# Kernel tuning notes

Hardware: AMD Instinct MI355X
Metric: run time of the kernel (lower is better)

## Reference

```python
import jax, jax.numpy as jnp
import numpy as np

N_NODES = 50000
N_EDGES = 800000
INPUT_DIM = 128
HIDDEN = 128
EMB = 64
OUT_DIM = 4


def gcn_norm(src, dst, w, num_nodes):
    """PyG gcn_norm: add self-loops (fill 1.0), sym-normalize D^-1/2 A D^-1/2."""
    loop = jnp.arange(num_nodes)
    src = jnp.concatenate([src, loop])
    dst = jnp.concatenate([dst, loop])
    w = jnp.concatenate([w, jnp.ones(num_nodes, w.dtype)])
    deg = jax.ops.segment_sum(w, dst, num_segments=num_nodes)
    dinv = jnp.where(deg > 0, jax.lax.rsqrt(jnp.where(deg > 0, deg, 1.0)), 0.0)
    return src, dst, dinv[src] * w * dinv[dst]


def propagate(h, src, dst, norm, num_nodes):
    # gather-scale-scatter-add: out[dst] += norm * h[src]
    return jax.ops.segment_sum(norm[:, None] * h[src], dst, num_segments=num_nodes)


def setup_inputs() -> dict:
    key = jax.random.key(0)
    ks = jax.random.split(key, 16)
    x = jax.random.normal(ks[0], (N_NODES, INPUT_DIM), dtype=jnp.float32)
    edge_index = jax.random.randint(ks[1], (2, N_EDGES), 0, N_NODES)
    edge_in = jax.random.randint(ks[2], (2, N_EDGES), 0, N_NODES)
    edge_out = jax.random.randint(ks[3], (2, N_EDGES), 0, N_NODES)
    in_w = jax.random.uniform(ks[4], (N_EDGES,), dtype=jnp.float32)
    out_w = jax.random.uniform(ks[5], (N_EDGES,), dtype=jnp.float32)
    # linear weights (bias=False), torch Linear stores [out, in]
    W0 = jax.random.normal(ks[6], (HIDDEN, INPUT_DIM), dtype=jnp.float32) / np.sqrt(INPUT_DIM)
    W1 = jax.random.normal(ks[7], (HIDDEN, HIDDEN * 3), dtype=jnp.float32) / np.sqrt(HIDDEN * 3)
    W2 = jax.random.normal(ks[8], (EMB, HIDDEN * 3), dtype=jnp.float32) / np.sqrt(HIDDEN * 3)
    b0 = jax.random.normal(ks[9], (1, HIDDEN), dtype=jnp.float32) * 0.01
    b1 = jax.random.normal(ks[10], (1, HIDDEN), dtype=jnp.float32) * 0.01
    b2 = jax.random.normal(ks[11], (1, EMB), dtype=jnp.float32) * 0.01
    # Conv1d(emb*3 -> out_dim, kernel=1) == pointwise linear
    Wc = jax.random.normal(ks[12], (OUT_DIM, EMB * 3), dtype=jnp.float32) / np.sqrt(EMB * 3)
    bc = jax.random.normal(ks[13], (OUT_DIM,), dtype=jnp.float32) * 0.01
    return {"x": x, "edge_index": edge_index, "edge_in": edge_in, "edge_out": edge_out,
            "in_w": in_w, "out_w": out_w, "W0": W0, "W1": W1, "W2": W2,
            "b0": b0, "b1": b1, "b2": b2, "Wc": Wc, "bc": bc}


def reference(x, edge_index, edge_in, edge_out, in_w, out_w,
              W0, W1, W2, b0, b1, b2, Wc, bc):
    n = x.shape[0]
    ones_w = jnp.ones(edge_index.shape[1], x.dtype)
    g1 = gcn_norm(edge_index[0], edge_index[1], ones_w, n)
    g2 = gcn_norm(edge_in[0], edge_in[1], in_w, n)
    g3 = gcn_norm(edge_out[0], edge_out[1], out_w, n)
    for W, b in zip((W0, W1, W2), (b0, b1, b2)):
        h = x @ W.T                                   # [N, d]
        x1 = propagate(h, g1[0], g1[1], g1[2], n) + b
        x2 = propagate(h, g2[0], g2[1], g2[2], n) + b
        x3 = propagate(h, g3[0], g3[1], g3[2], n) + b
        x = jax.nn.relu(jnp.concatenate([x1, x2, x3], axis=-1))
    # dropout_prob=0.0 / eval mode -> identity
    y = x @ Wc.T + bc                                 # 1x1 Conv1d == linear over features
    return x, jax.nn.log_softmax(y, axis=1)
```

## Files before the change

### kernel.cpp

```cpp
#include <hip/hip_runtime.h>
#include <hip/hip_bf16.h>
#include <hip/hip_fp16.h>

constexpr int NN = 50000;
constexpr int NE = 800000;
constexpr int NP = 50176;
constexpr int CAP = 56;
constexpr int NBC = 3 * (NE / 256);

__device__ __forceinline__ unsigned short bf16rne(float f) {
    unsigned int u = __float_as_uint(f);
    unsigned int r = (u + 0x7FFFu + ((u >> 16) & 1u)) >> 16;
    return (unsigned short)r;
}
__device__ __forceinline__ float bf16tof(unsigned short s) {
    return __uint_as_float((unsigned int)s << 16);
}


template <int K, int M>
__device__ __forceinline__ void gemm_body(const float* __restrict__ X,
                                          const float* __restrict__ W,
                                          unsigned short* __restrict__ H,
                                          int row0, int t,
                                          float (*xs)[68], float (*ws)[M + 4]) {
    constexpr int BM = 64, KC = 32;
    constexpr int CG = M / 4;
    constexpr int RG = 256 / CG;
    constexpr int RPT = BM / RG;
    int col4 = t % CG;
    int rbase = (t / CG) * RPT;
    float acc[RPT][4];
#pragma unroll
    for (int i = 0; i < RPT; ++i)
#pragma unroll
        for (int j = 0; j < 4; ++j) acc[i][j] = 0.f;

    for (int k0 = 0; k0 < K; k0 += KC) {
#pragma unroll
        for (int i = 0; i < 2; ++i) {
            int fid = t + 256 * i;
            int row = fid >> 3, kq = fid & 7;
            int gr = row0 + row; if (gr > NN - 1) gr = NN - 1;
            float4 v = *(const float4*)&X[(size_t)gr * K + k0 + kq * 4];
            xs[kq * 4 + 0][row] = v.x;
            xs[kq * 4 + 1][row] = v.y;
            xs[kq * 4 + 2][row] = v.z;
            xs[kq * 4 + 3][row] = v.w;
        }
#pragma unroll
        for (int i = 0; i < M / 32; ++i) {
            int fid = t + 256 * i;
            int m = fid >> 3, kq = fid & 7;
            float4 v = *(const float4*)&W[(size_t)m * K + k0 + kq * 4];
            ws[kq * 4 + 0][m] = v.x;
            ws[kq * 4 + 1][m] = v.y;
            ws[kq * 4 + 2][m] = v.z;
            ws[kq * 4 + 3][m] = v.w;
        }
        __syncthreads();
#pragma unroll
        for (int kk = 0; kk < KC; ++kk) {
            float4 wv = *(const float4*)&ws[kk][col4 * 4];
            float wa[4] = {wv.x, wv.y, wv.z, wv.w};
#pragma unroll
            for (int rq = 0; rq < RPT / 4; ++rq) {
                float4 xv = *(const float4*)&xs[kk][rbase + rq * 4];
                float xa[4] = {xv.x, xv.y, xv.z, xv.w};
#pragma unroll
                for (int rr = 0; rr < 4; ++rr)
#pragma unroll
                    for (int c = 0; c < 4; ++c)
                        acc[rq * 4 + rr][c] += xa[rr] * wa[c];
            }
        }
        __syncthreads();
    }
#pragma unroll
    for (int i = 0; i < RPT; ++i) {
        int gr = row0 + rbase + i;
        if (gr < NN) {
            ushort4 v;
            v.x = bf16rne(acc[i][0]);
            v.y = bf16rne(acc[i][1]);
            v.z = bf16rne(acc[i][2]);
            v.w = bf16rne(acc[i][3]);
            *(ushort4*)&H[(size_t)gr * M + col4 * 4] = v;
        }
    }
}


__global__ __launch_bounds__(256) void k_count_gemm(
    const int* __restrict__ e0, const int* __restrict__ e1, const int* __restrict__ e2,
    const float* __restrict__ w1, const float* __restrict__ w2,
    unsigned long long* __restrict__ combo, unsigned int* __restrict__ csrp,
    const float* __restrict__ X, const float* __restrict__ W,
    unsigned short* __restrict__ H) {
    int bid = blockIdx.x;
    if (bid < NBC) {
        int g = bid / (NE / 256);
        int e = (bid % (NE / 256)) * 256 + threadIdx.x;
        const int* ep = (g == 0) ? e0 : (g == 1) ? e1 : e2;
        float w = (g == 0) ? 1.0f : (g == 1) ? w1[e] : w2[e];
        int src = ep[e];
        int dst = ep[NE + e];
        unsigned long long wfix = (unsigned long long)llrint((double)w * 4294967296.0);
        unsigned long long old = atomicAdd(&combo[g * NP + dst], (1ULL << 44) | wfix);
        unsigned int rk = (unsigned int)(old >> 44);
        unsigned int wq = (unsigned int)lrintf(w * 65535.0f);
        if (rk < (unsigned int)CAP)
            csrp[((size_t)g * NP + dst) * CAP + rk] = (unsigned int)src | (wq << 16);
    } else {
        __shared__ __align__(16) float xs[32][68];
        __shared__ __align__(16) float ws[32][132];
        gemm_body<128, 128>(X, W, H, (bid - NBC) * 64, threadIdx.x, xs, ws);
    }
}

__global__ __launch_bounds__(256) void k_dinv(const unsigned long long* __restrict__ combo,
                                              float* __restrict__ dinv) {
    int i = blockIdx.x * 256 + threadIdx.x;
    if (i >= 3 * NP) return;
    unsigned long long v = combo[i];
    double d = (double)(v & ((1ULL << 44) - 1)) * (1.0 / 4294967296.0) + 1.0;
    dinv[i] = (float)(1.0 / sqrt(d));
}


__global__ __launch_bounds__(256) void k_nrm(unsigned int* __restrict__ csrp,
                                             const unsigned long long* __restrict__ combo,
                                             const float* __restrict__ dinv) {
    int node_g = blockIdx.x * 4 + (threadIdx.x >> 6);
    int l = threadIdx.x & 63;
    int cnt = (int)(combo[node_g] >> 44);
    if (cnt > CAP) cnt = CAP;
    if (l >= cnt) return;
    int g = node_g / NP;
    unsigned int* slot = csrp + (size_t)node_g * CAP + l;
    unsigned int v = *slot;
    unsigned int src = v & 0xFFFFu;
    float w = (float)(v >> 16) * (1.0f / 65535.0f);
    float nrm = dinv[g * NP + (int)src] * w * dinv[node_g];
    *slot = src | ((unsigned int)__half_as_ushort(__float2half(nrm)) << 16);
}


template <int K, int M>
__global__ __launch_bounds__(256) void k_gemm(const float* __restrict__ X,
                                              const float* __restrict__ W,
                                              unsigned short* __restrict__ H) {
    __shared__ __align__(16) float xs[32][68];
    __shared__ __align__(16) float ws[32][M + 4];
    gemm_body<K, M>(X, W, H, blockIdx.x * 64, threadIdx.x, xs, ws);
}


template <int D>
__global__ __launch_bounds__(256) void k_prop(const unsigned short* __restrict__ h,
                                              const unsigned int* __restrict__ csrp,
                                              const unsigned long long* __restrict__ combo,
                                              const float* __restrict__ dinv,
                                              const float* __restrict__ bias,
                                              float* __restrict__ xout) {
    constexpr int TPN = D / 4;
    constexpr int NPB = 256 / TPN;
    constexpr int UW = 8;
    int g = blockIdx.y;
    int node = blockIdx.x * NPB + threadIdx.x / TPN;
    int j4 = (threadIdx.x % TPN) * 4;
    if (node >= NN) return;
    int node_g = g * NP + node;
    int cnt = (int)(combo[node_g] >> 44);
    if (cnt > CAP) cnt = CAP;
    const unsigned int* row = csrp + (size_t)node_g * CAP;
    float dv = dinv[node_g];
    float sn = dv * dv;
    ushort4 hs = *(const ushort4*)&h[(size_t)node * D + j4];
    float4 acc = make_float4(sn * bf16tof(hs.x), sn * bf16tof(hs.y),
                             sn * bf16tof(hs.z), sn * bf16tof(hs.w));
    for (int e = 0; e < cnt; e += UW) {
        unsigned int v[UW];
        float nrm[UW];
#pragma unroll
        for (int i = 0; i < UW; ++i) {
            bool valid = (e + i) < cnt;
            v[i] = row[valid ? (e + i) : 0];
            nrm[i] = valid ? __half2float(__ushort_as_half((unsigned short)(v[i] >> 16))) : 0.f;
        }
        ushort4 hg[UW];
#pragma unroll
        for (int i = 0; i < UW; ++i)
            hg[i] = *(const ushort4*)&h[(size_t)(v[i] & 0xFFFFu) * D + j4];
#pragma unroll
        for (int i = 0; i < UW; ++i) {
            acc.x += nrm[i] * bf16tof(hg[i].x);
            acc.y += nrm[i] * bf16tof(hg[i].y);
            acc.z += nrm[i] * bf16tof(hg[i].z);
            acc.w += nrm[i] * bf16tof(hg[i].w);
        }
    }
    float4 bv = *(const float4*)&bias[j4];
    float4 r = make_float4(acc.x + bv.x, acc.y + bv.y, acc.z + bv.z, acc.w + bv.w);
    r.x = r.x > 0.f ? r.x : 0.f;
    r.y = r.y > 0.f ? r.y : 0.f;
    r.z = r.z > 0.f ? r.z : 0.f;
    r.w = r.w > 0.f ? r.w : 0.f;
    *(float4*)&xout[(size_t)node * (3 * D) + g * D + j4] = r;
}


__global__ __launch_bounds__(256) void k_final(const float* __restrict__ x,
                                               const float* __restrict__ Wc,
                                               const float* __restrict__ bc,
                                               float* __restrict__ out) {
    __shared__ __align__(16) float wl[4 * 192];
    __shared__ float bl[4];
    for (int i = threadIdx.x; i < 4 * 192; i += 256) wl[i] = Wc[i];
    if (threadIdx.x < 4) bl[threadIdx.x] = bc[threadIdx.x];
    __syncthreads();
    int node = blockIdx.x * 256 + threadIdx.x;
    if (node >= NN) return;
    const float4* xr = (const float4*)(x + (size_t)node * 192);
    float a[4] = {bl[0], bl[1], bl[2], bl[3]};
#pragma unroll
    for (int q = 0; q < 48; ++q) {
        float4 xv = xr[q];
#pragma unroll
        for (int o = 0; o < 4; ++o) {
            float4 wv = *(const float4*)&wl[o * 192 + q * 4];
            a[o] += xv.x * wv.x + xv.y * wv.y + xv.z * wv.z + xv.w * wv.w;
        }
    }
    float m = fmaxf(fmaxf(a[0], a[1]), fmaxf(a[2], a[3]));
    float s = expf(a[0] - m) + expf(a[1] - m) + expf(a[2] - m) + expf(a[3] - m);
    float ls = logf(s);
    *(float4*)&out[(size_t)node * 4] =
        make_float4(a[0] - m - ls, a[1] - m - ls, a[2] - m - ls, a[3] - m - ls);
}


extern "C" void kernel_launch(void* const* d_in, const int* in_sizes, int n_in,
                              void* d_out, int out_size, void* d_ws, size_t ws_size,
                              hipStream_t stream) {
    const float* x0 = (const float*)d_in[0];
    const int* e0 = (const int*)d_in[1];
    const int* e1 = (const int*)d_in[2];
    const int* e2 = (const int*)d_in[3];
    const float* w1 = (const float*)d_in[4];
    const float* w2 = (const float*)d_in[5];
    const float* W0 = (const float*)d_in[6];
    const float* W1 = (const float*)d_in[7];
    const float* W2 = (const float*)d_in[8];
    const float* b0 = (const float*)d_in[9];
    const float* b1 = (const float*)d_in[10];
    const float* b2 = (const float*)d_in[11];
    const float* Wc = (const float*)d_in[12];
    const float* bc = (const float*)d_in[13];
    float* out = (float*)d_out;

    char* wp = (char*)d_ws;
    auto alloc = [&](size_t bytes) -> void* {
        void* p = (void*)wp;
        wp += (bytes + 255) & ~(size_t)255;
        return p;
    };
    unsigned long long* combo = (unsigned long long*)alloc((size_t)3 * NP * 8);
    float*          dinv = (float*)alloc((size_t)3 * NP * 4);
    unsigned int*   csrp = (unsigned int*)alloc((size_t)3 * NP * CAP * 4);
    unsigned short* hbuf = (unsigned short*)alloc((size_t)NN * 128 * 2);
    float*          xA   = (float*)alloc((size_t)NN * 384 * 4);

    hipMemsetAsync(combo, 0, (size_t)3 * NP * 8, stream);
    k_count_gemm<<<NBC + (NN + 63) / 64, 256, 0, stream>>>(
        e0, e1, e2, w1, w2, combo, csrp, x0, W0, hbuf);
    k_dinv<<<(3 * NP + 255) / 256, 256, 0, stream>>>(combo, dinv);
    k_nrm<<<(3 * NP) / 4, 256, 0, stream>>>(csrp, combo, dinv);

    k_prop<128><<<dim3((NN + 7) / 8, 3), 256, 0, stream>>>(hbuf, csrp, combo, dinv, b0, xA);
    k_gemm<384, 128><<<(NN + 63) / 64, 256, 0, stream>>>(xA, W1, hbuf);
    k_prop<128><<<dim3((NN + 7) / 8, 3), 256, 0, stream>>>(hbuf, csrp, combo, dinv, b1, xA);
    k_gemm<384, 64><<<(NN + 63) / 64, 256, 0, stream>>>(xA, W2, hbuf);
    k_prop<64><<<dim3((NN + 15) / 16, 3), 256, 0, stream>>>(hbuf, csrp, combo, dinv, b2, out);
    k_final<<<(NN + 255) / 256, 256, 0, stream>>>(out, Wc, bc, out + (size_t)NN * 192);
}
```

Baseline: 669.7 us.

## Replace FP32 SIMT GEMMs with split-bf16 MFMA GEMMs

```diff
diff --git a/kernel.cpp b/kernel.cpp
--- a/kernel.cpp
+++ b/kernel.cpp
@@ -8,6 +8,9 @@
 constexpr int CAP = 56;
 constexpr int NBC = 3 * (NE / 256);
 
+typedef __attribute__((ext_vector_type(8))) short short8v;
+typedef __attribute__((ext_vector_type(4))) float f32x4;
+
 __device__ __forceinline__ unsigned short bf16rne(float f) {
     unsigned int u = __float_as_uint(f);
     unsigned int r = (u + 0x7FFFu + ((u >> 16) & 1u)) >> 16;
@@ -18,76 +21,82 @@
 }
 
 
+__global__ __launch_bounds__(256) void k_wsplit(
+    const float* __restrict__ W0, const float* __restrict__ W1, const float* __restrict__ W2,
+    unsigned short* __restrict__ h0, unsigned short* __restrict__ l0,
+    unsigned short* __restrict__ h1, unsigned short* __restrict__ l1,
+    unsigned short* __restrict__ h2, unsigned short* __restrict__ l2) {
+    int i = blockIdx.x * 256 + threadIdx.x;
+    const float* src; unsigned short *dh, *dl; int j;
+    if (i < 16384)       { src = W0; dh = h0; dl = l0; j = i; }
+    else if (i < 65536)  { src = W1; dh = h1; dl = l1; j = i - 16384; }
+    else if (i < 90112)  { src = W2; dh = h2; dl = l2; j = i - 65536; }
+    else return;
+    float v = src[j];
+    unsigned short hi = bf16rne(v);
+    dh[j] = hi;
+    dl[j] = bf16rne(v - bf16tof(hi));
+}
+
+
 template <int K, int M>
-__device__ __forceinline__ void gemm_body(const float* __restrict__ X,
-                                          const float* __restrict__ W,
-                                          unsigned short* __restrict__ H,
-                                          int row0, int t,
-                                          float (*xs)[68], float (*ws)[M + 4]) {
-    constexpr int BM = 64, KC = 32;
-    constexpr int CG = M / 4;
-    constexpr int RG = 256 / CG;
-    constexpr int RPT = BM / RG;
-    int col4 = t % CG;
-    int rbase = (t / CG) * RPT;
-    float acc[RPT][4];
-#pragma unroll
-    for (int i = 0; i < RPT; ++i)
-#pragma unroll
-        for (int j = 0; j < 4; ++j) acc[i][j] = 0.f;
-
-    for (int k0 = 0; k0 < K; k0 += KC) {
+__device__ __forceinline__ void gemm_mfma_body(
+    const float* __restrict__ X,
+    const unsigned short* __restrict__ Whi, const unsigned short* __restrict__ Wlo,
+    unsigned short* __restrict__ H, int row0, int t,
+    unsigned short (*xhi)[40], unsigned short (*xlo)[40],
+    unsigned short (*whi)[40], unsigned short (*wlo)[40]) {
+    constexpr int MT = M / 16;
+    int w = t >> 6, l = t & 63;
+    int la = l & 15, lb = l >> 4;
+    f32x4 acc[MT];
+#pragma unroll
+    for (int m = 0; m < MT; ++m) acc[m] = (f32x4){0.f, 0.f, 0.f, 0.f};
+
+    for (int k0 = 0; k0 < K; k0 += 32) {
 #pragma unroll
         for (int i = 0; i < 2; ++i) {
             int fid = t + 256 * i;
             int row = fid >> 3, kq = fid & 7;
             int gr = row0 + row; if (gr > NN - 1) gr = NN - 1;
             float4 v = *(const float4*)&X[(size_t)gr * K + k0 + kq * 4];
-            xs[kq * 4 + 0][row] = v.x;
-            xs[kq * 4 + 1][row] = v.y;
-            xs[kq * 4 + 2][row] = v.z;
-            xs[kq * 4 + 3][row] = v.w;
-        }
-#pragma unroll
-        for (int i = 0; i < M / 32; ++i) {
+            unsigned short h[4], lo[4];
+            float vv[4] = {v.x, v.y, v.z, v.w};
+#pragma unroll
+            for (int c = 0; c < 4; ++c) {
+                h[c] = bf16rne(vv[c]);
+                lo[c] = bf16rne(vv[c] - bf16tof(h[c]));
+            }
+            *(ulong1*)&xhi[row][kq * 4] = *(ulong1*)h;
+            *(ulong1*)&xlo[row][kq * 4] = *(ulong1*)lo;
+        }
+#pragma unroll
+        for (int i = 0; i < M / 64; ++i) {
             int fid = t + 256 * i;
-            int m = fid >> 3, kq = fid & 7;
-            float4 v = *(const float4*)&W[(size_t)m * K + k0 + kq * 4];
-            ws[kq * 4 + 0][m] = v.x;
-            ws[kq * 4 + 1][m] = v.y;
-            ws[kq * 4 + 2][m] = v.z;
-            ws[kq * 4 + 3][m] = v.w;
+            int m = fid >> 2, kq = fid & 3;
+            *(uint4*)&whi[m][kq * 8] = *(const uint4*)&Whi[(size_t)m * K + k0 + kq * 8];
+            *(uint4*)&wlo[m][kq * 8] = *(const uint4*)&Wlo[(size_t)m * K + k0 + kq * 8];
         }
         __syncthreads();
-#pragma unroll
-        for (int kk = 0; kk < KC; ++kk) {
-            float4 wv = *(const float4*)&ws[kk][col4 * 4];
-            float wa[4] = {wv.x, wv.y, wv.z, wv.w};
-#pragma unroll
-            for (int rq = 0; rq < RPT / 4; ++rq) {
-                float4 xv = *(const float4*)&xs[kk][rbase + rq * 4];
-                float xa[4] = {xv.x, xv.y, xv.z, xv.w};
-#pragma unroll
-                for (int rr = 0; rr < 4; ++rr)
-#pragma unroll
-                    for (int c = 0; c < 4; ++c)
-                        acc[rq * 4 + rr][c] += xa[rr] * wa[c];
-            }
+        short8v a_hi = *(const short8v*)&xhi[w * 16 + la][lb * 8];
+        short8v a_lo = *(const short8v*)&xlo[w * 16 + la][lb * 8];
+#pragma unroll
+        for (int m = 0; m < MT; ++m) {
+            short8v b_hi = *(const short8v*)&whi[m * 16 + la][lb * 8];
+            short8v b_lo = *(const short8v*)&wlo[m * 16 + la][lb * 8];
+            acc[m] = __builtin_amdgcn_mfma_f32_16x16x32_bf16(a_hi, b_hi, acc[m], 0, 0, 0);
+            acc[m] = __builtin_amdgcn_mfma_f32_16x16x32_bf16(a_hi, b_lo, acc[m], 0, 0, 0);
+            acc[m] = __builtin_amdgcn_mfma_f32_16x16x32_bf16(a_lo, b_hi, acc[m], 0, 0, 0);
         }
         __syncthreads();
     }
 #pragma unroll
-    for (int i = 0; i < RPT; ++i) {
-        int gr = row0 + rbase + i;
-        if (gr < NN) {
-            ushort4 v;
-            v.x = bf16rne(acc[i][0]);
-            v.y = bf16rne(acc[i][1]);
-            v.z = bf16rne(acc[i][2]);
-            v.w = bf16rne(acc[i][3]);
-            *(ushort4*)&H[(size_t)gr * M + col4 * 4] = v;
-        }
-    }
+    for (int m = 0; m < MT; ++m)
+#pragma unroll
+        for (int r = 0; r < 4; ++r) {
+            int gr = row0 + w * 16 + lb * 4 + r;
+            if (gr < NN) H[(size_t)gr * M + m * 16 + la] = bf16rne(acc[m][r]);
+        }
 }
 
 
@@ -95,7 +104,8 @@
     const int* __restrict__ e0, const int* __restrict__ e1, const int* __restrict__ e2,
     const float* __restrict__ w1, const float* __restrict__ w2,
     unsigned long long* __restrict__ combo, unsigned int* __restrict__ csrp,
-    const float* __restrict__ X, const float* __restrict__ W,
+    const float* __restrict__ X,
+    const unsigned short* __restrict__ Whi, const unsigned short* __restrict__ Wlo,
     unsigned short* __restrict__ H) {
     int bid = blockIdx.x;
     if (bid < NBC) {
@@ -112,9 +122,10 @@
         if (rk < (unsigned int)CAP)
             csrp[((size_t)g * NP + dst) * CAP + rk] = (unsigned int)src | (wq << 16);
     } else {
-        __shared__ __align__(16) float xs[32][68];
-        __shared__ __align__(16) float ws[32][132];
-        gemm_body<128, 128>(X, W, H, (bid - NBC) * 64, threadIdx.x, xs, ws);
+        __shared__ __align__(16) unsigned short xhi[64][40], xlo[64][40];
+        __shared__ __align__(16) unsigned short whi[128][40], wlo[128][40];
+        gemm_mfma_body<128, 128>(X, Whi, Wlo, H, (bid - NBC) * 64, threadIdx.x,
+                                 xhi, xlo, whi, wlo);
     }
 }
 
@@ -147,12 +158,13 @@
 
 
 template <int K, int M>
-__global__ __launch_bounds__(256) void k_gemm(const float* __restrict__ X,
-                                              const float* __restrict__ W,
-                                              unsigned short* __restrict__ H) {
-    __shared__ __align__(16) float xs[32][68];
-    __shared__ __align__(16) float ws[32][M + 4];
-    gemm_body<K, M>(X, W, H, blockIdx.x * 64, threadIdx.x, xs, ws);
+__global__ __launch_bounds__(256) void k_gemm_mfma(
+    const float* __restrict__ X,
+    const unsigned short* __restrict__ Whi, const unsigned short* __restrict__ Wlo,
+    unsigned short* __restrict__ H) {
+    __shared__ __align__(16) unsigned short xhi[64][40], xlo[64][40];
+    __shared__ __align__(16) unsigned short whi[M][40], wlo[M][40];
+    gemm_mfma_body<K, M>(X, Whi, Wlo, H, blockIdx.x * 64, threadIdx.x, xhi, xlo, whi, wlo);
 }
 
 
@@ -270,17 +282,24 @@
     unsigned int*   csrp = (unsigned int*)alloc((size_t)3 * NP * CAP * 4);
     unsigned short* hbuf = (unsigned short*)alloc((size_t)NN * 128 * 2);
     float*          xA   = (float*)alloc((size_t)NN * 384 * 4);
+    unsigned short* w0h  = (unsigned short*)alloc(16384 * 2);
+    unsigned short* w0l  = (unsigned short*)alloc(16384 * 2);
+    unsigned short* w1h  = (unsigned short*)alloc(49152 * 2);
+    unsigned short* w1l  = (unsigned short*)alloc(49152 * 2);
+    unsigned short* w2h  = (unsigned short*)alloc(24576 * 2);
+    unsigned short* w2l  = (unsigned short*)alloc(24576 * 2);
 
     hipMemsetAsync(combo, 0, (size_t)3 * NP * 8, stream);
+    k_wsplit<<<352, 256, 0, stream>>>(W0, W1, W2, w0h, w0l, w1h, w1l, w2h, w2l);
     k_count_gemm<<<NBC + (NN + 63) / 64, 256, 0, stream>>>(
-        e0, e1, e2, w1, w2, combo, csrp, x0, W0, hbuf);
+        e0, e1, e2, w1, w2, combo, csrp, x0, w0h, w0l, hbuf);
     k_dinv<<<(3 * NP + 255) / 256, 256, 0, stream>>>(combo, dinv);
     k_nrm<<<(3 * NP) / 4, 256, 0, stream>>>(csrp, combo, dinv);
 
     k_prop<128><<<dim3((NN + 7) / 8, 3), 256, 0, stream>>>(hbuf, csrp, combo, dinv, b0, xA);
-    k_gemm<384, 128><<<(NN + 63) / 64, 256, 0, stream>>>(xA, W1, hbuf);
+    k_gemm_mfma<384, 128><<<(NN + 63) / 64, 256, 0, stream>>>(xA, w1h, w1l, hbuf);
     k_prop<128><<<dim3((NN + 7) / 8, 3), 256, 0, stream>>>(hbuf, csrp, combo, dinv, b1, xA);
-    k_gemm<384, 64><<<(NN + 63) / 64, 256, 0, stream>>>(xA, W2, hbuf);
+    k_gemm_mfma<384, 64><<<(NN + 63) / 64, 256, 0, stream>>>(xA, w2h, w2l, hbuf);
     k_prop<64><<<dim3((NN + 15) / 16, 3), 256, 0, stream>>>(hbuf, csrp, combo, dinv, b2, out);
     k_final<<<(NN + 255) / 256, 256, 0, stream>>>(out, Wc, bc, out + (size_t)NN * 192);
 }
```

After: 581.8 us. 13.1% less time.
